# Kernel optimization log

Hardware: AMD Instinct MI355X
Metric: run time of the kernel (lower is better)

Reference implementation:

```python
import jax, jax.numpy as jnp
import numpy as np

B, S, D = 2, 2048, 2048
H = 16
HD = D // H
SCALE = 1.0 / (HD ** 0.5)


def setup_inputs() -> dict:
    key = jax.random.key(0)
    ks = jax.random.split(key, 9)
    std = 0.02
    return {
        "x": jax.random.normal(ks[0], (B, S, D), dtype=jnp.float32),
        "q_w": jax.random.normal(ks[1], (D, D), dtype=jnp.float32) * std,
        "q_b": jax.random.normal(ks[2], (D,), dtype=jnp.float32) * std,
        "k_w": jax.random.normal(ks[3], (D, D), dtype=jnp.float32) * std,
        "k_b": jax.random.normal(ks[4], (D,), dtype=jnp.float32) * std,
        "v_w": jax.random.normal(ks[5], (D, D), dtype=jnp.float32) * std,
        "v_b": jax.random.normal(ks[6], (D,), dtype=jnp.float32) * std,
        "o_w": jax.random.normal(ks[7], (D, D), dtype=jnp.float32) * std,
        "o_b": jax.random.normal(ks[8], (D,), dtype=jnp.float32) * std,
    }


def reference(x, q_w, q_b, k_w, k_b, v_w, v_b, o_w, o_b):
    # torch Linear: y = x @ W.T + b  (weights stored [out, in])
    b, s, _ = x.shape
    dtype = x.dtype
    q = (x @ q_w.T + q_b).reshape(b, s, H, HD).transpose(0, 2, 1, 3)  # [B,H,S,HD]
    k = (x @ k_w.T + k_b).reshape(b, s, H, HD).transpose(0, 2, 1, 3)
    v = (x @ v_w.T + v_b).reshape(b, s, H, HD).transpose(0, 2, 1, 3)
    scores = jnp.einsum("bhqd,bhkd->bhqk", q, k) * SCALE  # [B,H,S,S]
    # causal mask: positions k > q get -inf (via triu(diagonal=1))
    causal = jnp.triu(jnp.ones((s, s), dtype=bool), k=1)
    scores = jnp.where(causal[None, None], -jnp.inf, scores)
    attn = jax.nn.softmax(scores.astype(jnp.float32), axis=-1).astype(dtype)
    out = jnp.einsum("bhqk,bhkd->bhqd", attn, v)  # [B,H,S,HD]
    out = out.transpose(0, 2, 1, 3).reshape(b, s, H * HD)
    return out @ o_w.T + o_b
```

## Files before the change

kernel.cpp:

```cpp
#include <hip/hip_runtime.h>
#include <hip/hip_bf16.h>

#define S_LEN 2048
#define DMODEL 2048
#define NH 16
#define HDIM 128
#define SCALE_F 0.08838834764831845f

typedef __attribute__((ext_vector_type(8))) short bf16x8;
typedef __attribute__((ext_vector_type(4))) float f32x4;

__device__ __forceinline__ unsigned short f2bf(float f) {
  unsigned int u = __float_as_uint(f);
  u += 0x7FFFu + ((u >> 16) & 1u);
  return (unsigned short)(u >> 16);
}

__device__ __forceinline__ void gload16(const void* g, void* l) {
  __builtin_amdgcn_global_load_lds(
      (const __attribute__((address_space(1))) unsigned int*)g,
      (__attribute__((address_space(3))) unsigned int*)l, 16, 0, 0);
}

__global__ __launch_bounds__(256) void cvt_all(
    const float* __restrict__ x, const float* __restrict__ qw,
    const float* __restrict__ kw, const float* __restrict__ vw,
    const float* __restrict__ ow, unsigned short* __restrict__ xb,
    unsigned short* __restrict__ wqkv, unsigned short* __restrict__ wo) {
  int i = blockIdx.x * blockDim.x + threadIdx.x;
  const float* src;
  unsigned short* dst;
  int off;
  if (i < 2097152) {
    src = x; dst = xb; off = i;
  } else {
    const int j = i - 2097152;
    const int wsel = j >> 20;
    off = j & 1048575;
    src = (wsel == 0) ? qw : (wsel == 1) ? kw : (wsel == 2) ? vw : ow;
    dst = (wsel == 0) ? wqkv
        : (wsel == 1) ? (wqkv + 4194304)
        : (wsel == 2) ? (wqkv + 8388608)
                      : wo;
  }
  const float4 v = *(const float4*)(src + (size_t)off * 4);
  ushort4 o;
  o.x = f2bf(v.x); o.y = f2bf(v.y); o.z = f2bf(v.z); o.w = f2bf(v.w);
  *(ushort4*)(dst + (size_t)off * 4) = o;
}

__device__ __forceinline__ void gemm_core_128x256(
    const unsigned short* __restrict__ Ag, const unsigned short* __restrict__ Wg,
    int m0, int n0, char* lds, int t, f32x4 (&acc)[4][4]) {
  const int lane = t & 63, w = t >> 6;
  const int wr = w >> 2, wc = w & 3;

#pragma unroll
  for (int mi = 0; mi < 4; ++mi)
#pragma unroll
    for (int nj = 0; nj < 4; ++nj)
#pragma unroll
      for (int e = 0; e < 4; ++e) acc[mi][nj][e] = 0.f;

  const int fr = lane & 15;
  const int sw16 = (((lane >> 4) ^ ((lane >> 1) & 3)) << 4);
  const int aRowBase = (wr * 64 + fr) * 64;
  const int bRowBase = (wc * 64 + fr) * 64;

  const int cg8 = (((t & 3) ^ ((t >> 3) & 3)) * 8);
  const unsigned short* sAbase = Ag + (m0 + (t >> 2)) * DMODEL + cg8;
  const unsigned short* sBbase0 = Wg + (n0 + (t >> 2)) * DMODEL + cg8;
  const unsigned short* sBbase1 = sBbase0 + 128 * DMODEL;
  char* dstW = lds + w * 1024;

#pragma unroll
  for (int T = 0; T < 2; ++T)
#pragma unroll
    for (int h = 0; h < 2; ++h) {
      const int koff = T * 64 + h * 32;
      const int aoff = T * 16384 + h * 8192;
      const int boff = 32768 + T * 32768 + h * 16384;
      gload16(sAbase + koff, dstW + aoff);
      gload16(sBbase0 + koff, dstW + boff);
      gload16(sBbase1 + koff, dstW + boff + 8192);
    }
  asm volatile("s_waitcnt vmcnt(0)" ::: "memory");
  __builtin_amdgcn_s_barrier();

#pragma unroll 1
  for (int it = 0; it < 16; ++it) {
#pragma unroll
    for (int ph = 0; ph < 4; ++ph) {
      const int rA = (ph >> 1) * 16384 + (ph & 1) * 8192;
      const int rB = 32768 + (ph >> 1) * 32768 + (ph & 1) * 16384;
      bf16x8 a[4], b[4];
#pragma unroll
      for (int mi = 0; mi < 4; ++mi)
        a[mi] = *(const bf16x8*)(lds + rA + aRowBase + mi * 1024 + sw16);
#pragma unroll
      for (int nj = 0; nj < 4; ++nj)
        b[nj] = *(const bf16x8*)(lds + rB + bRowBase + nj * 1024 + sw16);

      const int SB_[4] = {1, 0, 0, 1};
      const int SH_[4] = {1, 0, 1, 0};
      const int TO_[4] = {1, 2, 2, 3};
      if (!(ph == 0 && it == 0)) {
        const int Tc = (2 * it + TO_[ph]) & 31;
        const int koff = Tc * 64 + SH_[ph] * 32;
        const int aoff = SB_[ph] * 16384 + SH_[ph] * 8192;
        const int boff = 32768 + SB_[ph] * 32768 + SH_[ph] * 16384;
        gload16(sAbase + koff, dstW + aoff);
        gload16(sBbase0 + koff, dstW + boff);
        gload16(sBbase1 + koff, dstW + boff + 8192);
      }
      asm volatile("s_waitcnt vmcnt(6)" ::: "memory");
      __builtin_amdgcn_s_barrier();
      asm volatile("s_waitcnt lgkmcnt(0)" ::: "memory");
      __builtin_amdgcn_sched_barrier(0);
      __builtin_amdgcn_s_setprio(1);
#pragma unroll
      for (int mi = 0; mi < 4; ++mi)
#pragma unroll
        for (int nj = 0; nj < 4; ++nj)
          acc[mi][nj] = __builtin_amdgcn_mfma_f32_16x16x32_bf16(
              a[mi], b[nj], acc[mi][nj], 0, 0, 0);
      __builtin_amdgcn_s_setprio(0);
      __builtin_amdgcn_s_barrier();
    }
  }
}

__global__ __launch_bounds__(512, 1) void gemm_qkv(
    const unsigned short* __restrict__ A, const unsigned short* __restrict__ W,
    const float* __restrict__ qbias, const float* __restrict__ kbias,
    const float* __restrict__ vbias,
    unsigned short* __restrict__ qo, unsigned short* __restrict__ ko,
    unsigned short* __restrict__ vto) {
  extern __shared__ char lds[];
  const int t = threadIdx.x;
  const int swz = ((int)blockIdx.x & 7) * 96 + ((int)blockIdx.x >> 3);
  const int m0 = (swz & 31) * 128;
  const int n0 = (swz >> 5) * 256;

  f32x4 acc[4][4];
  gemm_core_128x256(A, W, m0, n0, lds, t, acc);

  const int lane = t & 63, w = t >> 6;
  const int wr = w >> 2, wc = w & 3;
  const int b_ = m0 >> 11;
  const int proj = n0 >> 11;
  const int nn_base = (n0 & 2047) + wc * 64;
  const float* bias = (proj == 0) ? qbias : ((proj == 1) ? kbias : vbias);
#pragma unroll
  for (int nj = 0; nj < 4; ++nj) {
    const int nn = nn_base + nj * 16 + (lane & 15);
    const int h = nn >> 7, hd = nn & 127;
    const float bv = bias[nn];
#pragma unroll
    for (int mi = 0; mi < 4; ++mi) {
      const int mrow = m0 + wr * 64 + mi * 16 + (lane >> 4) * 4;
      const int s = mrow & 2047;
      if (proj == 2) {
        unsigned short* dst = vto + ((b_ * NH + h) * HDIM + hd) * S_LEN + s;
        ushort4 pk;
        pk.x = f2bf(acc[mi][nj][0] + bv);
        pk.y = f2bf(acc[mi][nj][1] + bv);
        pk.z = f2bf(acc[mi][nj][2] + bv);
        pk.w = f2bf(acc[mi][nj][3] + bv);
        *(ushort4*)dst = pk;
      } else {
        unsigned short* dst =
            ((proj == 0) ? qo : ko) + ((b_ * NH + h) * S_LEN + s) * HDIM + hd;
#pragma unroll
        for (int r = 0; r < 4; r++) dst[r * HDIM] = f2bf(acc[mi][nj][r] + bv);
      }
    }
  }
}

__global__ __launch_bounds__(512, 1) void gemm_out(
    const unsigned short* __restrict__ A, const unsigned short* __restrict__ W,
    const float* __restrict__ bias, float* __restrict__ out) {
  extern __shared__ char lds[];
  const int t = threadIdx.x;
  const int swz = ((int)blockIdx.x & 7) * 32 + ((int)blockIdx.x >> 3);
  const int m0 = (swz & 31) * 128;
  const int n0 = (swz >> 5) * 256;

  f32x4 acc[4][4];
  gemm_core_128x256(A, W, m0, n0, lds, t, acc);

  const int lane = t & 63, w = t >> 6;
  const int wr = w >> 2, wc = w & 3;
#pragma unroll
  for (int nj = 0; nj < 4; ++nj) {
    const int n = n0 + wc * 64 + nj * 16 + (lane & 15);
    const float bv = bias[n];
#pragma unroll
    for (int mi = 0; mi < 4; ++mi) {
      const int mrow = m0 + wr * 64 + mi * 16 + (lane >> 4) * 4;
      float* dst = out + (size_t)mrow * DMODEL + n;
#pragma unroll
      for (int r = 0; r < 4; r++) dst[r * DMODEL] = acc[mi][nj][r] + bv;
    }
  }
}

__global__ __launch_bounds__(256, 2) void attn_fwd(
    const unsigned short* __restrict__ Q,
    const unsigned short* __restrict__ K,
    const unsigned short* __restrict__ VT,
    unsigned short* __restrict__ ctx) {
  __shared__ unsigned short Ks[2][64 * 128];
  __shared__ unsigned short Vs[2][128 * 64];
  __shared__ unsigned short Ps[4][16 * 64];
  const int t = threadIdx.x, lane = t & 63, w = t >> 6;
  const int bh = blockIdx.y;
  const unsigned short* Qb = Q + bh * (S_LEN * HDIM);
  const unsigned short* Kb = K + bh * (S_LEN * HDIM);
  const unsigned short* Vb = VT + bh * (HDIM * S_LEN);
  const int b_ = bh >> 4, h = bh & 15;

  auto stageKV = [&](int buf, int kv0) {
#pragma unroll
    for (int u = 0; u < 4; ++u) {
      const int c = t + u * 256;
      const int row = c >> 4, cc = c & 15;
      gload16(Kb + (kv0 + row) * HDIM + ((cc ^ (row & 7)) * 8),
              (char*)Ks[buf] + u * 4096 + w * 1024);
    }
#pragma unroll
    for (int u = 0; u < 4; ++u) {
      const int c = t + u * 256;
      const int row = c >> 3, cc = c & 7;
      gload16(Vb + row * S_LEN + kv0 + ((cc ^ (row & 7)) * 8),
              (char*)Vs[buf] + u * 4096 + w * 1024);
    }
  };

#pragma unroll 1
  for (int pi = 0; pi < 2; ++pi) {
    const int qtile = pi ? (31 - blockIdx.x) : blockIdx.x;
    const int q0 = qtile * 64 + w * 16;

    bf16x8 qf[4];
    {
      const unsigned short* qrow =
          Qb + (q0 + (lane & 15)) * HDIM + (lane >> 4) * 8;
#pragma unroll
      for (int dk = 0; dk < 4; dk++) qf[dk] = *(const bf16x8*)(qrow + dk * 32);
    }

    float mrow[4], lrow[4];
    f32x4 oacc[8];
#pragma unroll
    for (int r = 0; r < 4; r++) { mrow[r] = -__builtin_inff(); lrow[r] = 0.f; }
#pragma unroll
    for (int d = 0; d < 8; d++)
#pragma unroll
      for (int e = 0; e < 4; e++) oacc[d][e] = 0.f;

    const int nt = qtile + 1;
    stageKV(0, 0);
    __syncthreads();
    int cur = 0;

#pragma unroll 1
    for (int kt = 0; kt < nt; ++kt) {
      if (kt + 1 < nt) stageKV(cur ^ 1, (kt + 1) * 64);

      const unsigned short* Kc = Ks[cur];
      const unsigned short* Vc = Vs[cur];
      const int kv0 = kt * 64;

      f32x4 sacc[4];
#pragma unroll
      for (int ck = 0; ck < 4; ck++)
#pragma unroll
        for (int e = 0; e < 4; e++) sacc[ck][e] = 0.f;
      __builtin_amdgcn_s_setprio(1);
#pragma unroll
      for (int ck = 0; ck < 4; ++ck) {
        const int krow = ck * 16 + (lane & 15);
#pragma unroll
        for (int dk = 0; dk < 4; ++dk) {
          const int chunk = dk * 4 + (lane >> 4);
          const bf16x8 kf = *(const bf16x8*)((const char*)Kc + krow * 256 +
                                             ((chunk ^ (krow & 7)) << 4));
          sacc[ck] = __builtin_amdgcn_mfma_f32_16x16x32_bf16(qf[dk], kf,
                                                             sacc[ck], 0, 0, 0);
        }
      }
      __builtin_amdgcn_s_setprio(0);
#pragma unroll
      for (int ck = 0; ck < 4; ck++)
#pragma unroll
        for (int r = 0; r < 4; r++) sacc[ck][r] *= SCALE_F;
      if (kt == qtile) {
#pragma unroll
        for (int ck = 0; ck < 4; ck++) {
          const int col = kv0 + ck * 16 + (lane & 15);
#pragma unroll
          for (int r = 0; r < 4; r++) {
            const int rowq = q0 + (lane >> 4) * 4 + r;
            if (col > rowq) sacc[ck][r] = -__builtin_inff();
          }
        }
      }
      float tmax[4];
#pragma unroll
      for (int r = 0; r < 4; r++)
        tmax[r] = fmaxf(fmaxf(sacc[0][r], sacc[1][r]),
                        fmaxf(sacc[2][r], sacc[3][r]));
#pragma unroll
      for (int off = 1; off < 16; off <<= 1)
#pragma unroll
        for (int r = 0; r < 4; r++)
          tmax[r] = fmaxf(tmax[r], __shfl_xor(tmax[r], off, 64));
      bool need = false;
#pragma unroll
      for (int r = 0; r < 4; r++) need |= (tmax[r] > mrow[r] + 8.f);
      if (__any(need)) {
#pragma unroll
        for (int r = 0; r < 4; r++) {
          const float mn = fmaxf(mrow[r], tmax[r]);
          const float corr = __expf(mrow[r] - mn);
          mrow[r] = mn;
          lrow[r] *= corr;
#pragma unroll
          for (int d = 0; d < 8; d++) oacc[d][r] *= corr;
        }
      }
      float rsum[4] = {0.f, 0.f, 0.f, 0.f};
#pragma unroll
      for (int ck = 0; ck < 4; ck++)
#pragma unroll
        for (int r = 0; r < 4; r++) {
          const float p = __expf(sacc[ck][r] - mrow[r]);
          rsum[r] += p;
          const int prow = (lane >> 4) * 4 + r;
          const int pcol = ck * 16 + (lane & 15);
          *(unsigned short*)((char*)Ps[w] +
                             ((prow * 128 + pcol * 2) ^ ((prow & 7) << 4))) =
              f2bf(p);
        }
#pragma unroll
      for (int off = 1; off < 16; off <<= 1)
#pragma unroll
        for (int r = 0; r < 4; r++) rsum[r] += __shfl_xor(rsum[r], off, 64);
#pragma unroll
      for (int r = 0; r < 4; r++) lrow[r] += rsum[r];

      bf16x8 pf[2];
      {
        const int prow = lane & 15;
#pragma unroll
        for (int kk = 0; kk < 2; kk++) {
          const int chunk = kk * 4 + (lane >> 4);
          pf[kk] = *(const bf16x8*)((const char*)Ps[w] + prow * 128 +
                                    ((chunk ^ (prow & 7)) << 4));
        }
      }
      __builtin_amdgcn_s_setprio(1);
#pragma unroll
      for (int d = 0; d < 8; ++d) {
        const int vrow = d * 16 + (lane & 15);
#pragma unroll
        for (int kk = 0; kk < 2; ++kk) {
          const int chunk = kk * 4 + (lane >> 4);
          const bf16x8 vf = *(const bf16x8*)((const char*)Vc + vrow * 128 +
                                             ((chunk ^ (vrow & 7)) << 4));
          oacc[d] = __builtin_amdgcn_mfma_f32_16x16x32_bf16(pf[kk], vf, oacc[d],
                                                            0, 0, 0);
        }
      }
      __builtin_amdgcn_s_setprio(0);

      __syncthreads();
      cur ^= 1;
    }

#pragma unroll
    for (int r = 0; r < 4; r++) {
      const float inv = 1.f / lrow[r];
      const int srow = q0 + (lane >> 4) * 4 + r;
      unsigned short* dst =
          ctx + (b_ * S_LEN + srow) * DMODEL + h * HDIM + (lane & 15);
#pragma unroll
      for (int d = 0; d < 8; d++) dst[d * 16] = f2bf(oacc[d][r] * inv);
    }
  }
}

extern "C" void kernel_launch(void* const* d_in, const int* in_sizes, int n_in,
                              void* d_out, int out_size, void* d_ws,
                              size_t ws_size, hipStream_t stream) {
  const float* x  = (const float*)d_in[0];
  const float* qw = (const float*)d_in[1];
  const float* qb = (const float*)d_in[2];
  const float* kw = (const float*)d_in[3];
  const float* kb = (const float*)d_in[4];
  const float* vw = (const float*)d_in[5];
  const float* vb = (const float*)d_in[6];
  const float* ow = (const float*)d_in[7];
  const float* ob = (const float*)d_in[8];
  float* out = (float*)d_out;

  unsigned short* xb   = (unsigned short*)d_ws;
  unsigned short* wqkv = xb + (size_t)8388608;
  unsigned short* wo   = wqkv + (size_t)12582912;
  unsigned short* qt_  = wo + (size_t)4194304;
  unsigned short* kt_  = qt_ + (size_t)8388608;
  unsigned short* vt_  = kt_ + (size_t)8388608;
  unsigned short* ctx  = vt_ + (size_t)8388608;

  cvt_all<<<24576, 256, 0, stream>>>(x, qw, kw, vw, ow, xb, wqkv, wo);

  gemm_qkv<<<768, 512, 98304, stream>>>(xb, wqkv, qb, kb, vb, qt_, kt_, vt_);
  attn_fwd<<<dim3(16, 32), 256, 0, stream>>>(qt_, kt_, vt_, ctx);
  gemm_out<<<256, 512, 98304, stream>>>(ctx, wo, ob, out);
}
```

Before: 283.7 us.

## Triple-buffer GEMM LDS stages to prefetch two k-tiles ahead

The shared GEMM core moves from a double-buffered LDS ring to a triple-buffered one. Loads now run two k-tiles ahead, and the wait points are relaxed so that only the older stage must land before each barrier. The main loop is restructured into groups of three tiles plus a drain tail, and LDS use grows from 96KB to 144KB per block. This is meant to hide more global-load latency behind MFMA work, at the cost of more LDS, and the explicit lgkmcnt wait and sched_barrier before the MFMAs are removed.

```diff
diff --git a/kernel.cpp b/kernel.cpp
--- a/kernel.cpp
+++ b/kernel.cpp
@@ -73,61 +73,59 @@
   const unsigned short* sBbase1 = sBbase0 + 128 * DMODEL;
   char* dstW = lds + w * 1024;
 
-#pragma unroll
-  for (int T = 0; T < 2; ++T)
-#pragma unroll
-    for (int h = 0; h < 2; ++h) {
-      const int koff = T * 64 + h * 32;
-      const int aoff = T * 16384 + h * 8192;
-      const int boff = 32768 + T * 32768 + h * 16384;
-      gload16(sAbase + koff, dstW + aoff);
-      gload16(sBbase0 + koff, dstW + boff);
-      gload16(sBbase1 + koff, dstW + boff + 8192);
-    }
-  asm volatile("s_waitcnt vmcnt(0)" ::: "memory");
+  auto stage3 = [&](int Tc, int h, int buf) {
+    const int koff = Tc * 64 + h * 32;
+    gload16(sAbase + koff, dstW + buf * 16384 + h * 8192);
+    gload16(sBbase0 + koff, dstW + 49152 + buf * 32768 + h * 16384);
+    gload16(sBbase1 + koff, dstW + 49152 + buf * 32768 + h * 16384 + 8192);
+  };
+
+  auto phase = [&](int h, int bufR, int doStage, int TS, int bufS, int vm) {
+    const int rA = bufR * 16384 + h * 8192;
+    const int rB = 49152 + bufR * 32768 + h * 16384;
+    bf16x8 a[4], b[4];
+#pragma unroll
+    for (int mi = 0; mi < 4; ++mi)
+      a[mi] = *(const bf16x8*)(lds + rA + aRowBase + mi * 1024 + sw16);
+#pragma unroll
+    for (int nj = 0; nj < 4; ++nj)
+      b[nj] = *(const bf16x8*)(lds + rB + bRowBase + nj * 1024 + sw16);
+    if (doStage) stage3(TS, h, bufS);
+    if (vm == 6) asm volatile("s_waitcnt vmcnt(6)" ::: "memory");
+    if (vm == 0) asm volatile("s_waitcnt vmcnt(0)" ::: "memory");
+    __builtin_amdgcn_s_barrier();
+    __builtin_amdgcn_s_setprio(1);
+#pragma unroll
+    for (int mi = 0; mi < 4; ++mi)
+#pragma unroll
+      for (int nj = 0; nj < 4; ++nj)
+        acc[mi][nj] = __builtin_amdgcn_mfma_f32_16x16x32_bf16(
+            a[mi], b[nj], acc[mi][nj], 0, 0, 0);
+    __builtin_amdgcn_s_setprio(0);
+    __builtin_amdgcn_s_barrier();
+  };
+
+  stage3(0, 0, 0);
+  stage3(0, 1, 0);
+  stage3(1, 0, 1);
+  stage3(1, 1, 1);
+  asm volatile("s_waitcnt vmcnt(6)" ::: "memory");
   __builtin_amdgcn_s_barrier();
 
 #pragma unroll 1
-  for (int it = 0; it < 16; ++it) {
-#pragma unroll
-    for (int ph = 0; ph < 4; ++ph) {
-      const int rA = (ph >> 1) * 16384 + (ph & 1) * 8192;
-      const int rB = 32768 + (ph >> 1) * 32768 + (ph & 1) * 16384;
-      bf16x8 a[4], b[4];
-#pragma unroll
-      for (int mi = 0; mi < 4; ++mi)
-        a[mi] = *(const bf16x8*)(lds + rA + aRowBase + mi * 1024 + sw16);
-#pragma unroll
-      for (int nj = 0; nj < 4; ++nj)
-        b[nj] = *(const bf16x8*)(lds + rB + bRowBase + nj * 1024 + sw16);
-
-      const int SB_[4] = {1, 0, 0, 1};
-      const int SH_[4] = {1, 0, 1, 0};
-      const int TO_[4] = {1, 2, 2, 3};
-      if (!(ph == 0 && it == 0)) {
-        const int Tc = (2 * it + TO_[ph]) & 31;
-        const int koff = Tc * 64 + SH_[ph] * 32;
-        const int aoff = SB_[ph] * 16384 + SH_[ph] * 8192;
-        const int boff = 32768 + SB_[ph] * 32768 + SH_[ph] * 16384;
-        gload16(sAbase + koff, dstW + aoff);
-        gload16(sBbase0 + koff, dstW + boff);
-        gload16(sBbase1 + koff, dstW + boff + 8192);
-      }
-      asm volatile("s_waitcnt vmcnt(6)" ::: "memory");
-      __builtin_amdgcn_s_barrier();
-      asm volatile("s_waitcnt lgkmcnt(0)" ::: "memory");
-      __builtin_amdgcn_sched_barrier(0);
-      __builtin_amdgcn_s_setprio(1);
-#pragma unroll
-      for (int mi = 0; mi < 4; ++mi)
-#pragma unroll
-        for (int nj = 0; nj < 4; ++nj)
-          acc[mi][nj] = __builtin_amdgcn_mfma_f32_16x16x32_bf16(
-              a[mi], b[nj], acc[mi][nj], 0, 0, 0);
-      __builtin_amdgcn_s_setprio(0);
-      __builtin_amdgcn_s_barrier();
-    }
+  for (int k3 = 0; k3 < 10; ++k3) {
+    const int T = k3 * 3;
+    phase(0, 0, 1, T + 2, 2, -1);
+    phase(1, 0, 1, T + 2, 2, 6);
+    phase(0, 1, 1, T + 3, 0, -1);
+    phase(1, 1, 1, T + 3, 0, 6);
+    phase(0, 2, 1, T + 4, 1, -1);
+    phase(1, 2, 1, T + 4, 1, 6);
   }
+  phase(0, 0, 0, 0, 0, -1);
+  phase(1, 0, 0, 0, 0, 0);
+  phase(0, 1, 0, 0, 0, -1);
+  phase(1, 1, 0, 0, 0, -1);
 }
 
 __global__ __launch_bounds__(512, 1) void gemm_qkv(
@@ -416,7 +414,7 @@
 
   cvt_all<<<24576, 256, 0, stream>>>(x, qw, kw, vw, ow, xb, wqkv, wo);
 
-  gemm_qkv<<<768, 512, 98304, stream>>>(xb, wqkv, qb, kb, vb, qt_, kt_, vt_);
+  gemm_qkv<<<768, 512, 147456, stream>>>(xb, wqkv, qb, kb, vb, qt_, kt_, vt_);
   attn_fwd<<<dim3(16, 32), 256, 0, stream>>>(qt_, kt_, vt_, ctx);
-  gemm_out<<<256, 512, 98304, stream>>>(ctx, wo, ob, out);
-}
+  gemm_out<<<256, 512, 147456, stream>>>(ctx, wo, ob, out);
+}
```

Result: no change. 279.9 us (-1.4%).
